# Performance work log

Measured on AMD Instinct MI355X. Metric: run time of the kernel, lower is better.

## Reference

```python
import jax, jax.numpy as jnp
import numpy as np

M = 150        # AR2 tail-fit window
LAM = 1e-3     # ridge regularizer in the 2x2 solve
CLIP_K = 4.0   # soft clip multiplier
H = 96         # forecast horizon (base_model.H)


def setup_inputs() -> dict:
    key = jax.random.key(0)
    k1, k2 = jax.random.split(key)
    x = jax.random.normal(k1, (32, 512, 2048), dtype=jnp.float32)
    W = jax.random.normal(k2, (2048, 96), dtype=jnp.float32) * 0.02
    return {"x": x, "W": W}


def _ar2_forecast(x):
    # x: (B, C, L); closed-form AR2 fit on last M samples, vectorized over (B, C)
    y = x[..., -M:]                     # (B, C, M)
    Y = y[..., 2:]                      # targets
    p1 = y[..., 1:-1]
    p2 = y[..., :-2]
    s = lambda a, b: jnp.sum(a * b, axis=-1)
    A11 = s(p1, p1) + LAM
    A22 = s(p2, p2) + LAM
    A12 = s(p1, p2)
    b1 = s(p1, Y)
    b2 = s(p2, Y)
    det = A11 * A22 - A12 * A12
    a1 = (b1 * A22 - b2 * A12) / det    # (B, C)
    a2 = (A11 * b2 - A12 * b1) / det

    def step(carry, _):
        y1, y2 = carry
        yn = a1 * y1 + a2 * y2
        return (yn, y1), yn

    _, out = jax.lax.scan(step, (x[..., -1], x[..., -2]), None, length=H)
    return jnp.moveaxis(out, 0, -1)     # (B, C, H)


def reference(x, W):
    # AR2 part is computed on detached history in the original (numpy round-trip)
    Yb = jax.lax.stop_gradient(_ar2_forecast(x))
    d_hat = jnp.einsum('bcl,lh->bch', x, W)          # base model: per-channel linear head
    y_hat = Yb + d_hat
    last = x[..., -1:]                               # (B, C, 1), broadcasts over H
    hstd = jnp.maximum(jnp.std(x, axis=-1, ddof=1, keepdims=True), 1e-6)  # torch unbiased std
    return jnp.clip(y_hat, last - CLIP_K * hstd, last + CLIP_K * hstd)
```

## Files before the change

### kernel.cpp

```cpp
#include <hip/hip_runtime.h>
#include <math.h>

constexpr int L     = 2048;
constexpr int NH    = 96;
constexpr int MLEN  = 150;
constexpr int NAR   = 148;
constexpr float LAM    = 0.001f;
constexpr float CLIP_K = 4.0f;

constexpr int TM     = 16;
constexpr int KM     = 64;
constexpr int MSTEPS = L / KM;
constexpr int NBUF   = 4;

typedef __attribute__((ext_vector_type(8))) short short8;
typedef __attribute__((ext_vector_type(4))) float floatx4;

__device__ inline short f2bf(float f) {
    union { float f; unsigned u; } v; v.f = f;
    unsigned r = v.u + 0x7FFFu + ((v.u >> 16) & 1u);
    return (short)(r >> 16);
}

__global__ __launch_bounds__(256) void wt_kernel(
    const float* __restrict__ W, short* __restrict__ Wt)
{
    int idx = blockIdx.x * 256 + threadIdx.x;
    int n = idx >> 11;
    int k = idx & 2047;
    Wt[idx] = f2bf(W[k * NH + n]);
}

__global__ __launch_bounds__(256, 2) void gemm_ar2_kernel(
    const float* __restrict__ x, const short* __restrict__ Wt,
    float* __restrict__ out)
{
    __shared__ float As[NBUF][TM * KM];
    __shared__ short Bs[NBUF][NH * KM];
    __shared__ float Ys[TM][NH + 1];
    __shared__ float los[TM], his[TM];
    __shared__ float s2[TM], q2[TM];

    const int t    = threadIdx.x;
    const int lane = t & 63;
    const int wv   = t >> 6;
    const int g    = wv & 1;
    const int e    = wv >> 1;
    const int m    = lane & 15;
    const int quad = lane >> 4;
    const int row0 = blockIdx.x * TM;

    const int rA = t >> 4, chA = t & 15;
    const float* pa = x + (size_t)(row0 + rA) * L
                        + ((chA >> 3) * 32 + ((chA & 7) ^ (rA & 7)) * 4);

    const int cB0 = wv * 192 + lane, cB1 = cB0 + 64, cB2 = cB0 + 128;
    const short* pb0 = Wt + (size_t)(cB0 >> 3) * L + (((cB0 & 7) ^ ((cB0 >> 3) & 7)) * 8);
    const short* pb1 = Wt + (size_t)(cB1 >> 3) * L + (((cB1 & 7) ^ ((cB1 >> 3) & 7)) * 8);
    const short* pb2 = Wt + (size_t)(cB2 >> 3) * L + (((cB2 & 7) ^ ((cB2 >> 3) & 7)) * 8);

    floatx4 acc[3];
    #pragma unroll
    for (int jj = 0; jj < 3; ++jj) acc[jj] = floatx4{0.f, 0.f, 0.f, 0.f};
    float sum = 0.f, sumsq = 0.f;

    const int pA0 = (2 * quad)     ^ (m & 7);
    const int pA1 = (2 * quad + 1) ^ (m & 7);

    auto stage = [&](int buf, int k0) {
        __builtin_amdgcn_global_load_lds(
            (const __attribute__((address_space(1))) unsigned int*)(pa + k0),
            (__attribute__((address_space(3))) unsigned int*)&As[buf][wv * 256], 16, 0, 0);
        __builtin_amdgcn_global_load_lds(
            (const __attribute__((address_space(1))) unsigned int*)(pb0 + k0),
            (__attribute__((address_space(3))) unsigned int*)&Bs[buf][wv * 1536], 16, 0, 0);
        __builtin_amdgcn_global_load_lds(
            (const __attribute__((address_space(1))) unsigned int*)(pb1 + k0),
            (__attribute__((address_space(3))) unsigned int*)&Bs[buf][wv * 1536 + 512], 16, 0, 0);
        __builtin_amdgcn_global_load_lds(
            (const __attribute__((address_space(1))) unsigned int*)(pb2 + k0),
            (__attribute__((address_space(3))) unsigned int*)&Bs[buf][wv * 1536 + 1024], 16, 0, 0);
    };

    stage(0, 0);
    stage(1, KM);
    stage(2, 2 * KM);

    for (int s = 0; s < MSTEPS; ++s) {
        const int cur = s & 3;
        if (s < MSTEPS - 3) {
            asm volatile("s_waitcnt vmcnt(8)" ::: "memory");
            __builtin_amdgcn_s_barrier();
            asm volatile("" ::: "memory");
            stage((s + 3) & 3, (s + 3) * KM);
        } else {
            __syncthreads();
        }

        float4 f0 = *(const float4*)&As[cur][m * KM + e * 32 + pA0 * 4];
        float4 f1 = *(const float4*)&As[cur][m * KM + e * 32 + pA1 * 4];

        if (g == 0) {
            sum  += ((f0.x + f0.y) + (f0.z + f0.w))
                  + ((f1.x + f1.y) + (f1.z + f1.w));
            sumsq = fmaf(f0.x, f0.x, sumsq); sumsq = fmaf(f0.y, f0.y, sumsq);
            sumsq = fmaf(f0.z, f0.z, sumsq); sumsq = fmaf(f0.w, f0.w, sumsq);
            sumsq = fmaf(f1.x, f1.x, sumsq); sumsq = fmaf(f1.y, f1.y, sumsq);
            sumsq = fmaf(f1.z, f1.z, sumsq); sumsq = fmaf(f1.w, f1.w, sumsq);
        }

        short8 af;
        af[0] = f2bf(f0.x); af[1] = f2bf(f0.y); af[2] = f2bf(f0.z); af[3] = f2bf(f0.w);
        af[4] = f2bf(f1.x); af[5] = f2bf(f1.y); af[6] = f2bf(f1.z); af[7] = f2bf(f1.w);

        const int bch = ((e * 4 + quad) ^ (m & 7)) * 8;
        #pragma unroll
        for (int jj = 0; jj < 3; ++jj) {
            short8 bf = *(const short8*)&Bs[cur][(g * 48 + jj * 16 + m) * KM + bch];
            acc[jj] = __builtin_amdgcn_mfma_f32_16x16x32_bf16(af, bf, acc[jj], 0, 0, 0);
        }
    }

    float* ar = (float*)&Bs[0][0];
    if (e == 1) {
        #pragma unroll
        for (int jj = 0; jj < 3; ++jj)
            #pragma unroll
            for (int reg = 0; reg < 4; ++reg)
                ar[(g * 64 + lane) * 12 + jj * 4 + reg] = acc[jj][reg];
        if (g == 0) {
            float su = sum, sq = sumsq;
            su += __shfl_xor(su, 16); su += __shfl_xor(su, 32);
            sq += __shfl_xor(sq, 16); sq += __shfl_xor(sq, 32);
            if (quad == 0) { s2[m] = su; q2[m] = sq; }
        }
    }
    __syncthreads();

    if (e == 0) {
        #pragma unroll
        for (int jj = 0; jj < 3; ++jj)
            #pragma unroll
            for (int reg = 0; reg < 4; ++reg)
                acc[jj][reg] += ar[(g * 64 + lane) * 12 + jj * 4 + reg];

        if (g == 0) {
            sum   += __shfl_xor(sum,   16); sum   += __shfl_xor(sum,   32);
            sumsq += __shfl_xor(sumsq, 16); sumsq += __shfl_xor(sumsq, 32);

            const float* ytail = x + (size_t)(row0 + m) * L + (L - MLEN);
            float A11 = 0.f, A22 = 0.f, A12 = 0.f, b1 = 0.f, b2 = 0.f;
            for (int i = quad; i < NAR; i += 4) {
                float p2v = ytail[i];
                float p1v = ytail[i + 1];
                float Yv  = ytail[i + 2];
                A11 = fmaf(p1v, p1v, A11);
                A22 = fmaf(p2v, p2v, A22);
                A12 = fmaf(p1v, p2v, A12);
                b1  = fmaf(p1v, Yv,  b1);
                b2  = fmaf(p2v, Yv,  b2);
            }
            A11 += __shfl_xor(A11, 16); A11 += __shfl_xor(A11, 32);
            A22 += __shfl_xor(A22, 16); A22 += __shfl_xor(A22, 32);
            A12 += __shfl_xor(A12, 16); A12 += __shfl_xor(A12, 32);
            b1  += __shfl_xor(b1,  16); b1  += __shfl_xor(b1,  32);
            b2  += __shfl_xor(b2,  16); b2  += __shfl_xor(b2,  32);

            if (quad == 0) {
                sum   += s2[m];
                sumsq += q2[m];
                A11 += LAM; A22 += LAM;
                float det = A11 * A22 - A12 * A12;
                float a1c = (b1 * A22 - b2 * A12) / det;
                float a2c = (A11 * b2 - A12 * b1) / det;

                float last = ytail[MLEN - 1];
                float y1 = last;
                float y2 = ytail[MLEN - 2];
                for (int n = 0; n < NH; ++n) {
                    float yn = a1c * y1 + a2c * y2;
                    Ys[m][n] = yn;
                    y2 = y1; y1 = yn;
                }
                float var  = (sumsq - sum * sum * (1.0f / L)) * (1.0f / (L - 1));
                float hstd = fmaxf(sqrtf(fmaxf(var, 0.f)), 1e-6f);
                los[m] = last - CLIP_K * hstd;
                his[m] = last + CLIP_K * hstd;
            }
        }
    }
    __syncthreads();

    if (e == 0) {
        #pragma unroll
        for (int reg = 0; reg < 4; ++reg) {
            int rl = quad * 4 + reg;
            float lo = los[rl], hi = his[rl];
            #pragma unroll
            for (int jj = 0; jj < 3; ++jj) {
                int c = (3 * g + jj) * 16 + m;
                float v = acc[jj][reg] + Ys[rl][c];
                v = fminf(fmaxf(v, lo), hi);
                out[(size_t)(row0 + rl) * NH + c] = v;
            }
        }
    }
}

extern "C" void kernel_launch(void* const* d_in, const int* in_sizes, int n_in,
                              void* d_out, int out_size, void* d_ws, size_t ws_size,
                              hipStream_t stream) {
    const float* x = (const float*)d_in[0];
    const float* W = (const float*)d_in[1];
    float* out = (float*)d_out;
    short* Wt  = (short*)d_ws;

    wt_kernel<<<dim3((NH * L) / 256), dim3(256), 0, stream>>>(W, Wt);

    const int rows = 32 * 512;
    gemm_ar2_kernel<<<dim3(rows / TM), dim3(256), 0, stream>>>(x, Wt, out);
}
```

Measured before the change: 228.9 us.

## Load W fragments straight to registers, drop B LDS staging, raise occupancy

The bf16 weight tile is no longer staged through shared memory. Each lane loads its MFMA B fragment directly from global memory into registers, one step ahead of use, while only the x tile still goes through LDS via global_load_lds. This removes the B LDS buffers and their reads, which shrinks shared memory per block so the launch bound can allow 4 blocks per CU. The costs are more global load traffic per wave through L2 (the same B data is fetched by every block into registers), more register pressure, and new vmcnt wait counts that must match the mixed load stream exactly.

```diff
diff --git a/kernel.cpp b/kernel.cpp
--- a/kernel.cpp
+++ b/kernel.cpp
@@ -31,12 +31,11 @@
     Wt[idx] = f2bf(W[k * NH + n]);
 }
 
-__global__ __launch_bounds__(256, 2) void gemm_ar2_kernel(
+__global__ __launch_bounds__(256, 4) void gemm_ar2_kernel(
     const float* __restrict__ x, const short* __restrict__ Wt,
     float* __restrict__ out)
 {
     __shared__ float As[NBUF][TM * KM];
-    __shared__ short Bs[NBUF][NH * KM];
     __shared__ float Ys[TM][NH + 1];
     __shared__ float los[TM], his[TM];
     __shared__ float s2[TM], q2[TM];
@@ -54,51 +53,55 @@
     const float* pa = x + (size_t)(row0 + rA) * L
                         + ((chA >> 3) * 32 + ((chA & 7) ^ (rA & 7)) * 4);
 
-    const int cB0 = wv * 192 + lane, cB1 = cB0 + 64, cB2 = cB0 + 128;
-    const short* pb0 = Wt + (size_t)(cB0 >> 3) * L + (((cB0 & 7) ^ ((cB0 >> 3) & 7)) * 8);
-    const short* pb1 = Wt + (size_t)(cB1 >> 3) * L + (((cB1 & 7) ^ ((cB1 >> 3) & 7)) * 8);
-    const short* pb2 = Wt + (size_t)(cB2 >> 3) * L + (((cB2 & 7) ^ ((cB2 >> 3) & 7)) * 8);
+    const short* pb0 = Wt + (size_t)(g * 48 + m) * L + e * 32 + quad * 8;
+    const short* pb1 = pb0 + 16 * (size_t)L;
+    const short* pb2 = pb0 + 32 * (size_t)L;
 
     floatx4 acc[3];
     #pragma unroll
     for (int jj = 0; jj < 3; ++jj) acc[jj] = floatx4{0.f, 0.f, 0.f, 0.f};
     float sum = 0.f, sumsq = 0.f;
 
-    const int pA0 = (2 * quad)     ^ (m & 7);
-    const int pA1 = (2 * quad + 1) ^ (m & 7);
-
-    auto stage = [&](int buf, int k0) {
+    const int pA0  = (2 * quad)     ^ (m & 7);
+    const int pA1  = (2 * quad + 1) ^ (m & 7);
+    const int aoff = m * KM + e * 32;
+
+    auto stageA = [&](int buf, int k0) {
         __builtin_amdgcn_global_load_lds(
             (const __attribute__((address_space(1))) unsigned int*)(pa + k0),
             (__attribute__((address_space(3))) unsigned int*)&As[buf][wv * 256], 16, 0, 0);
-        __builtin_amdgcn_global_load_lds(
-            (const __attribute__((address_space(1))) unsigned int*)(pb0 + k0),
-            (__attribute__((address_space(3))) unsigned int*)&Bs[buf][wv * 1536], 16, 0, 0);
-        __builtin_amdgcn_global_load_lds(
-            (const __attribute__((address_space(1))) unsigned int*)(pb1 + k0),
-            (__attribute__((address_space(3))) unsigned int*)&Bs[buf][wv * 1536 + 512], 16, 0, 0);
-        __builtin_amdgcn_global_load_lds(
-            (const __attribute__((address_space(1))) unsigned int*)(pb2 + k0),
-            (__attribute__((address_space(3))) unsigned int*)&Bs[buf][wv * 1536 + 1024], 16, 0, 0);
     };
 
-    stage(0, 0);
-    stage(1, KM);
-    stage(2, 2 * KM);
-
+    stageA(0, 0);
+    asm volatile("" ::: "memory");
+    short8 cb0 = *(const short8*)(pb0);
+    short8 cb1 = *(const short8*)(pb1);
+    short8 cb2 = *(const short8*)(pb2);
+    asm volatile("" ::: "memory");
+    stageA(1, KM);
+    stageA(2, 2 * KM);
+
+    #pragma unroll 4
     for (int s = 0; s < MSTEPS; ++s) {
         const int cur = s & 3;
-        if (s < MSTEPS - 3) {
-            asm volatile("s_waitcnt vmcnt(8)" ::: "memory");
+        if (s >= MSTEPS - 2) {
+            __syncthreads();
+        } else {
+            if (s >= 2) asm volatile("s_waitcnt vmcnt(8)" ::: "memory");
+            else        asm volatile("s_waitcnt vmcnt(5)" ::: "memory");
             __builtin_amdgcn_s_barrier();
-            asm volatile("" ::: "memory");
-            stage((s + 3) & 3, (s + 3) * KM);
-        } else {
-            __syncthreads();
-        }
-
-        float4 f0 = *(const float4*)&As[cur][m * KM + e * 32 + pA0 * 4];
-        float4 f1 = *(const float4*)&As[cur][m * KM + e * 32 + pA1 * 4];
+        }
+        __builtin_amdgcn_sched_barrier(0);
+
+        const int off = (s + 1 < MSTEPS ? s + 1 : s) * KM;
+        short8 nb0 = *(const short8*)(pb0 + off);
+        short8 nb1 = *(const short8*)(pb1 + off);
+        short8 nb2 = *(const short8*)(pb2 + off);
+        asm volatile("" ::: "memory");
+        if (s + 3 < MSTEPS) stageA((s + 3) & 3, (s + 3) * KM);
+
+        float4 f0 = *(const float4*)&As[cur][aoff + pA0 * 4];
+        float4 f1 = *(const float4*)&As[cur][aoff + pA1 * 4];
 
         if (g == 0) {
             sum  += ((f0.x + f0.y) + (f0.z + f0.w))
@@ -113,15 +116,14 @@
         af[0] = f2bf(f0.x); af[1] = f2bf(f0.y); af[2] = f2bf(f0.z); af[3] = f2bf(f0.w);
         af[4] = f2bf(f1.x); af[5] = f2bf(f1.y); af[6] = f2bf(f1.z); af[7] = f2bf(f1.w);
 
-        const int bch = ((e * 4 + quad) ^ (m & 7)) * 8;
-        #pragma unroll
-        for (int jj = 0; jj < 3; ++jj) {
-            short8 bf = *(const short8*)&Bs[cur][(g * 48 + jj * 16 + m) * KM + bch];
-            acc[jj] = __builtin_amdgcn_mfma_f32_16x16x32_bf16(af, bf, acc[jj], 0, 0, 0);
-        }
-    }
-
-    float* ar = (float*)&Bs[0][0];
+        acc[0] = __builtin_amdgcn_mfma_f32_16x16x32_bf16(af, cb0, acc[0], 0, 0, 0);
+        acc[1] = __builtin_amdgcn_mfma_f32_16x16x32_bf16(af, cb1, acc[1], 0, 0, 0);
+        acc[2] = __builtin_amdgcn_mfma_f32_16x16x32_bf16(af, cb2, acc[2], 0, 0, 0);
+
+        cb0 = nb0; cb1 = nb1; cb2 = nb2;
+    }
+
+    float* ar = (float*)&As[0][0];
     if (e == 1) {
         #pragma unroll
         for (int jj = 0; jj < 3; ++jj)
```

New measurement: 217.1 us. -5.1%, faster.
